# Kernel optimization log

Measured on AMD Instinct MI355X. Metric: run time of the kernel, lower is better.

The kernel has to match this reference:

```python
import jax, jax.numpy as jnp
import numpy as np

N_NODES = 100000
N_EDGES = 3200000
IN_DIM = 256
OUT_DIM = 128


def setup_inputs() -> dict:
    key = jax.random.key(0)
    k_x, k_w, k_r, k_c, k_v = jax.random.split(key, 5)
    X = jax.random.normal(k_x, (N_NODES, IN_DIM), dtype=jnp.float32)
    # kaiming_normal on [in, out]: fan computed along dim 1 -> std = sqrt(2/out)
    weight = jax.random.normal(k_w, (IN_DIM, OUT_DIM), dtype=jnp.float32) * np.sqrt(2.0 / OUT_DIM)
    bias = jnp.zeros((OUT_DIM,), dtype=jnp.float32)
    adj_rows = jax.random.randint(k_r, (N_EDGES,), 0, N_NODES, dtype=jnp.int32)
    adj_cols = jax.random.randint(k_c, (N_EDGES,), 0, N_NODES, dtype=jnp.int32)
    adj_vals = jax.random.uniform(k_v, (N_EDGES,), dtype=jnp.float32)
    return {"X": X, "weight": weight, "bias": bias,
            "adj_rows": adj_rows, "adj_cols": adj_cols, "adj_vals": adj_vals}


def reference(X, weight, bias, adj_rows, adj_cols, adj_vals):
    # support = X @ W  -> [N, out]
    support = jnp.matmul(X, weight)
    # SpMM: output[r] = sum_e vals[e] * support[cols[e]] for edges with rows[e]==r
    messages = adj_vals[:, None] * support[adj_cols]          # [E, out]
    output = jax.ops.segment_sum(messages, adj_rows, num_segments=N_NODES)
    return output + bias
```

## Files before the change

### kernel.cpp

```cpp
#include <hip/hip_runtime.h>

#define N_NODES 100000
#define N_EDGES 3200000
#define IN_DIM  256
#define OUT_DIM 128

#define CB      256
#define NCB     391
#define NB2     256
#define CHUNK2  12500
#define SCAN_N  (NCB * NB2)
#define SCAN_BS 1024
#define SCAN_NB ((SCAN_N + SCAN_BS - 1) / SCAN_BS)
#define LDSE    10240

#define GBM 128

typedef __attribute__((ext_vector_type(8))) short bf16x8;
typedef __attribute__((ext_vector_type(4))) float f32x4;

__device__ __forceinline__ unsigned short f2bf(float x) {
    unsigned u = __float_as_uint(x);
    unsigned r = (u + 0x7FFFu + ((u >> 16) & 1u)) >> 16;
    return (unsigned short)r;
}
__device__ __forceinline__ float bflo(unsigned d) { return __uint_as_float(d << 16); }
__device__ __forceinline__ float bfhi(unsigned d) { return __uint_as_float(d & 0xFFFF0000u); }

__global__ __launch_bounds__(256) void wtrans_kernel(const float* __restrict__ W,
                                                     unsigned short* __restrict__ WT) {
    const int n = blockIdx.x;
    const int k = threadIdx.x;
    WT[(size_t)n * IN_DIM + k] = f2bf(W[(size_t)k * OUT_DIM + n]);
}

__global__ __launch_bounds__(256) void gemm_mfma(const float* __restrict__ X,
                                                 const unsigned short* __restrict__ WT,
                                                 unsigned short* __restrict__ SH) {
    __shared__ char lds[32768];
    char* ldsX = lds;
    char* ldsW = lds + 16384;

    const int t    = threadIdx.x;
    const int row0 = blockIdx.x * GBM;
    const int w    = t >> 6;
    const int l    = t & 63;
    const int r16  = l & 15;
    const int kg   = l >> 4;

    f32x4 acc[2][8];
#pragma unroll
    for (int mr = 0; mr < 2; ++mr)
#pragma unroll
        for (int nc = 0; nc < 8; ++nc) acc[mr][nc] = (f32x4)(0.f);

    const int srow = t >> 1;
    const int sseg = t & 1;

    for (int k0 = 0; k0 < IN_DIM; k0 += 64) {
        {
            int grow = row0 + srow;
            bool live = grow < N_NODES;
            const float4* xp = (const float4*)(X + (size_t)(live ? grow : 0) * IN_DIM + k0 + sseg * 32);
#pragma unroll
            for (int c = 0; c < 4; ++c) {
                uint4 wv = make_uint4(0, 0, 0, 0);
                if (live) {
                    float4 fa = xp[c * 2], fb = xp[c * 2 + 1];
                    wv.x = (unsigned)f2bf(fa.x) | ((unsigned)f2bf(fa.y) << 16);
                    wv.y = (unsigned)f2bf(fa.z) | ((unsigned)f2bf(fa.w) << 16);
                    wv.z = (unsigned)f2bf(fb.x) | ((unsigned)f2bf(fb.y) << 16);
                    wv.w = (unsigned)f2bf(fb.z) | ((unsigned)f2bf(fb.w) << 16);
                }
                int byte = srow * 128 + (sseg * 32 + c * 8) * 2;
                byte ^= (srow & 7) << 4;
                *(uint4*)(ldsX + byte) = wv;
            }
            const uint4* wp = (const uint4*)(WT + (size_t)srow * IN_DIM + k0 + sseg * 32);
#pragma unroll
            for (int c = 0; c < 4; ++c) {
                uint4 wv = wp[c];
                int byte = srow * 128 + (sseg * 32 + c * 8) * 2;
                byte ^= (srow & 7) << 4;
                *(uint4*)(ldsW + byte) = wv;
            }
        }
        __syncthreads();

#pragma unroll
        for (int ks = 0; ks < 64; ks += 32) {
            bf16x8 af[2], bfr[8];
#pragma unroll
            for (int mr = 0; mr < 2; ++mr) {
                int row  = w * 32 + mr * 16 + r16;
                int byte = row * 128 + (ks + kg * 8) * 2;
                byte ^= (row & 7) << 4;
                af[mr] = *(const bf16x8*)(ldsX + byte);
            }
#pragma unroll
            for (int nc = 0; nc < 8; ++nc) {
                int n    = nc * 16 + r16;
                int byte = n * 128 + (ks + kg * 8) * 2;
                byte ^= (n & 7) << 4;
                bfr[nc] = *(const bf16x8*)(ldsW + byte);
            }
#pragma unroll
            for (int mr = 0; mr < 2; ++mr)
#pragma unroll
                for (int nc = 0; nc < 8; ++nc)
                    acc[mr][nc] = __builtin_amdgcn_mfma_f32_16x16x32_bf16(af[mr], bfr[nc], acc[mr][nc], 0, 0, 0);
        }
        __syncthreads();
    }

#pragma unroll
    for (int mr = 0; mr < 2; ++mr)
#pragma unroll
        for (int j = 0; j < 4; ++j) {
            int grow = row0 + w * 32 + mr * 16 + kg * 4 + j;
            if (grow < N_NODES) {
#pragma unroll
                for (int nc = 0; nc < 8; ++nc)
                    SH[(size_t)grow * OUT_DIM + nc * 16 + r16] = f2bf(acc[mr][nc][j]);
            }
        }
}

__global__ __launch_bounds__(1024) void pA_hist(const int* __restrict__ rows,
                                                int* __restrict__ gcounts) {
    __shared__ int hist[NCB];
    const int b = blockIdx.x, t = threadIdx.x;
    for (int k = t; k < NCB; k += 1024) hist[k] = 0;
    __syncthreads();
    const int beg = b * CHUNK2, end = beg + CHUNK2;
    for (int i = beg + t; i < end; i += 1024) atomicAdd(&hist[rows[i] >> 8], 1);
    __syncthreads();
    for (int k = t; k < NCB; k += 1024) gcounts[k * NB2 + b] = hist[k];
}

__global__ __launch_bounds__(256) void scan1_kernel(int* __restrict__ data,
                                                    int* __restrict__ bsums) {
    __shared__ int tsum[256];
    const int t    = threadIdx.x;
    const int base = blockIdx.x * SCAN_BS + t * 4;
    int v[4];
#pragma unroll
    for (int j = 0; j < 4; ++j) {
        int idx = base + j;
        v[j] = (idx < SCAN_N) ? data[idx] : 0;
    }
    tsum[t] = v[0] + v[1] + v[2] + v[3];
    __syncthreads();
    for (int off = 1; off < 256; off <<= 1) {
        int x = (t >= off) ? tsum[t - off] : 0;
        __syncthreads();
        tsum[t] += x;
        __syncthreads();
    }
    int run = (t == 0) ? 0 : tsum[t - 1];
#pragma unroll
    for (int j = 0; j < 4; ++j) {
        int idx = base + j;
        if (idx < SCAN_N) data[idx] = run;
        run += v[j];
    }
    if (t == 255) bsums[blockIdx.x] = tsum[255];
}

__global__ void scan2_kernel(int* __restrict__ bsums) {
    if (threadIdx.x == 0 && blockIdx.x == 0) {
        int run = 0;
        for (int i = 0; i < SCAN_NB; ++i) { int v = bsums[i]; bsums[i] = run; run += v; }
    }
}

__global__ __launch_bounds__(256) void scan3_kernel(int* __restrict__ data,
                                                    const int* __restrict__ bsums) {
    int i = blockIdx.x * 256 + threadIdx.x;
    if (i < SCAN_N) data[i] += bsums[i / SCAN_BS];
}

__global__ __launch_bounds__(1024) void pA_scatter(const int* __restrict__ rows,
                                                   const int* __restrict__ cols,
                                                   const float* __restrict__ vals,
                                                   const int* __restrict__ pscan,
                                                   uint2* __restrict__ sorted) {
    __shared__ int cursor[NCB];
    const int b = blockIdx.x, t = threadIdx.x;
    for (int k = t; k < NCB; k += 1024) cursor[k] = pscan[k * NB2 + b];
    __syncthreads();
    const int beg = b * CHUNK2, end = beg + CHUNK2;
    for (int i = beg + t; i < end; i += 1024) {
        int r   = rows[i];
        int k   = r >> 8;
        int pos = atomicAdd(&cursor[k], 1);
        sorted[pos] = make_uint2(__float_as_uint(vals[i]),
                                 ((unsigned)(r & (CB - 1)) << 17) | (unsigned)cols[i]);
    }
}

__global__ __launch_bounds__(1024) void pB_sort(uint2* __restrict__ sorted,
                                                const int* __restrict__ pscan,
                                                int* __restrict__ rstart2) {
    __shared__ uint2 ebuf[LDSE];
    __shared__ int cnt[CB];
    __shared__ int cur[CB];
    __shared__ int sbuf[2][CB];
    const int cb = blockIdx.x, t = threadIdx.x;
    const int beg = pscan[cb * NB2];
    const int end = (cb == NCB - 1) ? N_EDGES : pscan[(cb + 1) * NB2];
    const int n   = end - beg;
    const int nl  = (n < LDSE) ? n : LDSE;

    if (t < CB) cnt[t] = 0;
    __syncthreads();

    for (int i = t; i < n; i += 1024) {
        uint2 m = sorted[beg + i];
        if (i < LDSE) ebuf[i] = m;
        atomicAdd(&cnt[(m.y >> 17) & 255], 1);
    }
    __syncthreads();

    if (t < CB) sbuf[0][t] = cnt[t];
    __syncthreads();
    int p = 0;
    for (int off = 1; off < CB; off <<= 1) {
        if (t < CB) sbuf[p ^ 1][t] = sbuf[p][t] + ((t >= off) ? sbuf[p][t - off] : 0);
        __syncthreads();
        p ^= 1;
    }
    if (t < CB) {
        int excl = (t == 0) ? 0 : sbuf[p][t - 1];
        int gi   = cb * CB + t;
        if (gi <= N_NODES) rstart2[gi] = beg + excl;
        cur[t] = beg + excl;
    }
    uint2 ov[4];
    int nov = 0;
    for (int i = nl + t; i < n && nov < 4; i += 1024) ov[nov++] = sorted[beg + i];
    __syncthreads();

    for (int i = t; i < nl; i += 1024) {
        uint2 m  = ebuf[i];
        int rl   = (m.y >> 17) & 255;
        int pos  = atomicAdd(&cur[rl], 1);
        sorted[pos] = make_uint2(m.x, m.y & 0x1FFFFu);
    }
    for (int j = 0; j < nov; ++j) {
        uint2 m  = ov[j];
        int rl   = (m.y >> 17) & 255;
        int pos  = atomicAdd(&cur[rl], 1);
        sorted[pos] = make_uint2(m.x, m.y & 0x1FFFFu);
    }
}

__global__ __launch_bounds__(256) void p6_rowsum(const int* __restrict__ rstart2,
                                                 const uint2* __restrict__ sorted,
                                                 const unsigned short* __restrict__ SH,
                                                 const float* __restrict__ bias,
                                                 float* __restrict__ out) {
    const int wid  = (blockIdx.x * 256 + threadIdx.x) >> 6;
    const int lane = threadIdx.x & 63;
    if (wid >= N_NODES) return;

    const int beg = rstart2[wid];
    const int end = rstart2[wid + 1];
    const int qg  = lane >> 4;
    const int ql  = lane & 15;

    float a0 = 0.f, a1 = 0.f, a2 = 0.f, a3 = 0.f, a4 = 0.f, a5 = 0.f, a6 = 0.f, a7 = 0.f;

#define ACC8(vv, gg)                                     \
    {                                                    \
        a0 += (vv) * bflo((gg).x); a1 += (vv) * bfhi((gg).x); \
        a2 += (vv) * bflo((gg).y); a3 += (vv) * bfhi((gg).y); \
        a4 += (vv) * bflo((gg).z); a5 += (vv) * bfhi((gg).z); \
        a6 += (vv) * bflo((gg).w); a7 += (vv) * bfhi((gg).w); \
    }

    int i = beg;
    for (; i + 8 <= end; i += 8) {
        uint2 m0 = sorted[i + qg];
        uint2 m1 = sorted[i + 4 + qg];
        uint4 g0 = *(const uint4*)(SH + (size_t)m0.y * OUT_DIM + ql * 8);
        uint4 g1 = *(const uint4*)(SH + (size_t)m1.y * OUT_DIM + ql * 8);
        float v0 = __uint_as_float(m0.x);
        float v1 = __uint_as_float(m1.x);
        ACC8(v0, g0)
        ACC8(v1, g1)
    }
    for (; i < end; i += 4) {
        int  idx  = i + qg;
        int  cidx = (idx < end) ? idx : (end - 1);
        uint2 m   = sorted[cidx];
        float v   = (idx < end) ? __uint_as_float(m.x) : 0.f;
        uint4 g   = *(const uint4*)(SH + (size_t)m.y * OUT_DIM + ql * 8);
        ACC8(v, g)
    }
#undef ACC8

    a0 += __shfl_xor(a0, 16); a1 += __shfl_xor(a1, 16); a2 += __shfl_xor(a2, 16); a3 += __shfl_xor(a3, 16);
    a4 += __shfl_xor(a4, 16); a5 += __shfl_xor(a5, 16); a6 += __shfl_xor(a6, 16); a7 += __shfl_xor(a7, 16);
    a0 += __shfl_xor(a0, 32); a1 += __shfl_xor(a1, 32); a2 += __shfl_xor(a2, 32); a3 += __shfl_xor(a3, 32);
    a4 += __shfl_xor(a4, 32); a5 += __shfl_xor(a5, 32); a6 += __shfl_xor(a6, 32); a7 += __shfl_xor(a7, 32);

    if (lane < 16) {
        const float4* bp = (const float4*)bias + ql * 2;
        float4 b0 = bp[0], b1 = bp[1];
        float4* orow = (float4*)(out + (size_t)wid * OUT_DIM) + ql * 2;
        orow[0] = make_float4(a0 + b0.x, a1 + b0.y, a2 + b0.z, a3 + b0.w);
        orow[1] = make_float4(a4 + b1.x, a5 + b1.y, a6 + b1.z, a7 + b1.w);
    }
}

extern "C" void kernel_launch(void* const* d_in, const int* in_sizes, int n_in,
                              void* d_out, int out_size, void* d_ws, size_t ws_size,
                              hipStream_t stream) {
    const float* X    = (const float*)d_in[0];
    const float* W    = (const float*)d_in[1];
    const float* bias = (const float*)d_in[2];
    const int*   rows = (const int*)d_in[3];
    const int*   cols = (const int*)d_in[4];
    const float* vals = (const float*)d_in[5];
    float* out = (float*)d_out;

    char* ws = (char*)d_ws;
    unsigned short* SH      = (unsigned short*)ws;
    uint2*          sorted  = (uint2*)(ws + 25600000);
    int*            pscan   = (int*)(ws + 51200000);
    int*            rstart2 = (int*)(ws + 51600384);
    int*            bsums   = (int*)(ws + 52000768);
    unsigned short* WT      = (unsigned short*)(ws + 52001280);

    hipLaunchKernelGGL(wtrans_kernel, dim3(OUT_DIM), dim3(IN_DIM), 0, stream, W, WT);
    hipLaunchKernelGGL(gemm_mfma, dim3((N_NODES + GBM - 1) / GBM), dim3(256), 0, stream,
                       X, WT, SH);
    hipLaunchKernelGGL(pA_hist, dim3(NB2), dim3(1024), 0, stream, rows, pscan);
    hipLaunchKernelGGL(scan1_kernel, dim3(SCAN_NB), dim3(256), 0, stream, pscan, bsums);
    hipLaunchKernelGGL(scan2_kernel, dim3(1), dim3(64), 0, stream, bsums);
    hipLaunchKernelGGL(scan3_kernel, dim3((SCAN_N + 255) / 256), dim3(256), 0, stream,
                       pscan, bsums);
    hipLaunchKernelGGL(pA_scatter, dim3(NB2), dim3(1024), 0, stream,
                       rows, cols, vals, pscan, sorted);
    hipLaunchKernelGGL(pB_sort, dim3(NCB), dim3(1024), 0, stream,
                       sorted, pscan, rstart2);
    hipLaunchKernelGGL(p6_rowsum, dim3((N_NODES + 3) / 4), dim3(256), 0, stream,
                       rstart2, sorted, SH, bias, out);
}
```

Measured before the change: 221.3 us.

## Use nontemporal loads, packed bf16 convert, deeper gather unroll, fold scan2

```diff
diff --git a/kernel.cpp b/kernel.cpp
--- a/kernel.cpp
+++ b/kernel.cpp
@@ -18,11 +18,18 @@
 
 typedef __attribute__((ext_vector_type(8))) short bf16x8;
 typedef __attribute__((ext_vector_type(4))) float f32x4;
+typedef unsigned int u32x2 __attribute__((ext_vector_type(2)));
+typedef unsigned int u32x4 __attribute__((ext_vector_type(4)));
 
 __device__ __forceinline__ unsigned short f2bf(float x) {
     unsigned u = __float_as_uint(x);
     unsigned r = (u + 0x7FFFu + ((u >> 16) & 1u)) >> 16;
     return (unsigned short)r;
+}
+__device__ __forceinline__ unsigned cvtpk_bf16(float lo, float hi) {
+    unsigned r;
+    asm("v_cvt_pk_bf16_f32 %0, %1, %2" : "=v"(r) : "v"(lo), "v"(hi));
+    return r;
 }
 __device__ __forceinline__ float bflo(unsigned d) { return __uint_as_float(d << 16); }
 __device__ __forceinline__ float bfhi(unsigned d) { return __uint_as_float(d & 0xFFFF0000u); }
@@ -67,10 +74,10 @@
                 uint4 wv = make_uint4(0, 0, 0, 0);
                 if (live) {
                     float4 fa = xp[c * 2], fb = xp[c * 2 + 1];
-                    wv.x = (unsigned)f2bf(fa.x) | ((unsigned)f2bf(fa.y) << 16);
-                    wv.y = (unsigned)f2bf(fa.z) | ((unsigned)f2bf(fa.w) << 16);
-                    wv.z = (unsigned)f2bf(fb.x) | ((unsigned)f2bf(fb.y) << 16);
-                    wv.w = (unsigned)f2bf(fb.z) | ((unsigned)f2bf(fb.w) << 16);
+                    wv.x = cvtpk_bf16(fa.x, fa.y);
+                    wv.y = cvtpk_bf16(fa.z, fa.w);
+                    wv.z = cvtpk_bf16(fb.x, fb.y);
+                    wv.w = cvtpk_bf16(fb.z, fb.w);
                 }
                 int byte = srow * 128 + (sseg * 32 + c * 8) * 2;
                 byte ^= (srow & 7) << 4;
@@ -133,7 +140,10 @@
     for (int k = t; k < NCB; k += 1024) hist[k] = 0;
     __syncthreads();
     const int beg = b * CHUNK2, end = beg + CHUNK2;
-    for (int i = beg + t; i < end; i += 1024) atomicAdd(&hist[rows[i] >> 8], 1);
+    for (int i = beg + t; i < end; i += 1024) {
+        int r = __builtin_nontemporal_load(&rows[i]);
+        atomicAdd(&hist[r >> 8], 1);
+    }
     __syncthreads();
     for (int k = t; k < NCB; k += 1024) gcounts[k * NB2 + b] = hist[k];
 }
@@ -167,17 +177,13 @@
     if (t == 255) bsums[blockIdx.x] = tsum[255];
 }
 
-__global__ void scan2_kernel(int* __restrict__ bsums) {
-    if (threadIdx.x == 0 && blockIdx.x == 0) {
-        int run = 0;
-        for (int i = 0; i < SCAN_NB; ++i) { int v = bsums[i]; bsums[i] = run; run += v; }
-    }
-}
-
 __global__ __launch_bounds__(256) void scan3_kernel(int* __restrict__ data,
                                                     const int* __restrict__ bsums) {
     int i = blockIdx.x * 256 + threadIdx.x;
-    if (i < SCAN_N) data[i] += bsums[i / SCAN_BS];
+    int b = (blockIdx.x * 256) / SCAN_BS;
+    int pfx = 0;
+    for (int j = 0; j < b; ++j) pfx += bsums[j];
+    if (i < SCAN_N) data[i] += pfx;
 }
 
 __global__ __launch_bounds__(1024) void pA_scatter(const int* __restrict__ rows,
@@ -191,11 +197,13 @@
     __syncthreads();
     const int beg = b * CHUNK2, end = beg + CHUNK2;
     for (int i = beg + t; i < end; i += 1024) {
-        int r   = rows[i];
+        int   r = __builtin_nontemporal_load(&rows[i]);
+        int   c = __builtin_nontemporal_load(&cols[i]);
+        float v = __builtin_nontemporal_load(&vals[i]);
         int k   = r >> 8;
         int pos = atomicAdd(&cursor[k], 1);
-        sorted[pos] = make_uint2(__float_as_uint(vals[i]),
-                                 ((unsigned)(r & (CB - 1)) << 17) | (unsigned)cols[i]);
+        sorted[pos] = make_uint2(__float_as_uint(v),
+                                 ((unsigned)(r & (CB - 1)) << 17) | (unsigned)c);
     }
 }
 
@@ -269,10 +277,13 @@
     const int qg  = lane >> 4;
     const int ql  = lane & 15;
 
+    const u32x2* sp = (const u32x2*)sorted;
+
     float a0 = 0.f, a1 = 0.f, a2 = 0.f, a3 = 0.f, a4 = 0.f, a5 = 0.f, a6 = 0.f, a7 = 0.f;
 
-#define ACC8(vv, gg)                                     \
-    {                                                    \
+#define GATHER(mm) __builtin_nontemporal_load((const u32x4*)(SH + (size_t)(mm).y * OUT_DIM) + ql)
+#define ACC8(vv, gg)                                          \
+    {                                                         \
         a0 += (vv) * bflo((gg).x); a1 += (vv) * bfhi((gg).x); \
         a2 += (vv) * bflo((gg).y); a3 += (vv) * bfhi((gg).y); \
         a4 += (vv) * bflo((gg).z); a5 += (vv) * bfhi((gg).z); \
@@ -280,25 +291,41 @@
     }
 
     int i = beg;
-    for (; i + 8 <= end; i += 8) {
-        uint2 m0 = sorted[i + qg];
-        uint2 m1 = sorted[i + 4 + qg];
-        uint4 g0 = *(const uint4*)(SH + (size_t)m0.y * OUT_DIM + ql * 8);
-        uint4 g1 = *(const uint4*)(SH + (size_t)m1.y * OUT_DIM + ql * 8);
-        float v0 = __uint_as_float(m0.x);
-        float v1 = __uint_as_float(m1.x);
+    for (; i + 16 <= end; i += 16) {
+        u32x2 m0 = __builtin_nontemporal_load(sp + i + qg);
+        u32x2 m1 = __builtin_nontemporal_load(sp + i + 4 + qg);
+        u32x2 m2 = __builtin_nontemporal_load(sp + i + 8 + qg);
+        u32x2 m3 = __builtin_nontemporal_load(sp + i + 12 + qg);
+        u32x4 g0 = GATHER(m0);
+        u32x4 g1 = GATHER(m1);
+        u32x4 g2 = GATHER(m2);
+        u32x4 g3 = GATHER(m3);
+        float v0 = __uint_as_float(m0.x), v1 = __uint_as_float(m1.x);
+        float v2 = __uint_as_float(m2.x), v3 = __uint_as_float(m3.x);
         ACC8(v0, g0)
         ACC8(v1, g1)
+        ACC8(v2, g2)
+        ACC8(v3, g3)
+    }
+    for (; i + 8 <= end; i += 8) {
+        u32x2 m0 = __builtin_nontemporal_load(sp + i + qg);
+        u32x2 m1 = __builtin_nontemporal_load(sp + i + 4 + qg);
+        u32x4 g0 = GATHER(m0);
+        u32x4 g1 = GATHER(m1);
+        float v0 = __uint_as_float(m0.x), v1 = __uint_as_float(m1.x);
+        ACC8(v0, g0)
+        ACC8(v1, g1)
     }
     for (; i < end; i += 4) {
-        int  idx  = i + qg;
-        int  cidx = (idx < end) ? idx : (end - 1);
-        uint2 m   = sorted[cidx];
-        float v   = (idx < end) ? __uint_as_float(m.x) : 0.f;
-        uint4 g   = *(const uint4*)(SH + (size_t)m.y * OUT_DIM + ql * 8);
+        int   idx  = i + qg;
+        int   cidx = (idx < end) ? idx : (end - 1);
+        u32x2 m    = __builtin_nontemporal_load(sp + cidx);
+        float v    = (idx < end) ? __uint_as_float(m.x) : 0.f;
+        u32x4 g    = GATHER(m);
         ACC8(v, g)
     }
 #undef ACC8
+#undef GATHER
 
     a0 += __shfl_xor(a0, 16); a1 += __shfl_xor(a1, 16); a2 += __shfl_xor(a2, 16); a3 += __shfl_xor(a3, 16);
     a4 += __shfl_xor(a4, 16); a5 += __shfl_xor(a5, 16); a6 += __shfl_xor(a6, 16); a7 += __shfl_xor(a7, 16);
@@ -308,9 +335,11 @@
     if (lane < 16) {
         const float4* bp = (const float4*)bias + ql * 2;
         float4 b0 = bp[0], b1 = bp[1];
-        float4* orow = (float4*)(out + (size_t)wid * OUT_DIM) + ql * 2;
-        orow[0] = make_float4(a0 + b0.x, a1 + b0.y, a2 + b0.z, a3 + b0.w);
-        orow[1] = make_float4(a4 + b1.x, a5 + b1.y, a6 + b1.z, a7 + b1.w);
+        f32x4 o0 = {a0 + b0.x, a1 + b0.y, a2 + b0.z, a3 + b0.w};
+        f32x4 o1 = {a4 + b1.x, a5 + b1.y, a6 + b1.z, a7 + b1.w};
+        f32x4* orow = (f32x4*)(out + (size_t)wid * OUT_DIM) + ql * 2;
+        __builtin_nontemporal_store(o0, orow);
+        __builtin_nontemporal_store(o1, orow + 1);
     }
 }
 
@@ -338,7 +367,6 @@
                        X, WT, SH);
     hipLaunchKernelGGL(pA_hist, dim3(NB2), dim3(1024), 0, stream, rows, pscan);
     hipLaunchKernelGGL(scan1_kernel, dim3(SCAN_NB), dim3(256), 0, stream, pscan, bsums);
-    hipLaunchKernelGGL(scan2_kernel, dim3(1), dim3(64), 0, stream, bsums);
     hipLaunchKernelGGL(scan3_kernel, dim3((SCAN_N + 255) / 256), dim3(256), 0, stream,
                        pscan, bsums);
     hipLaunchKernelGGL(pA_scatter, dim3(NB2), dim3(1024), 0, stream,
```

Result: slower. 289.1 us (+30.7%).
